# Performance work log

Hardware: AMD Instinct MI355X
Metric: run time of the kernel (lower is better)

## Reference

```python
import jax, jax.numpy as jnp
import numpy as np
from jax import lax

C = 768
CA = C // 4  # adapter_channels = 192
L = 197      # 1 CLS + 14*14 patches
T_FRAMES = 16
B = 16
N = B * T_FRAMES


def quick_gelu(x):
    return x * jax.nn.sigmoid(1.702 * x)


def setup_inputs() -> dict:
    key = jax.random.key(0)
    ks = jax.random.split(key, 16)
    s = 0.02
    return {
        "x": jax.random.normal(ks[0], (L, N, C), dtype=jnp.float32),
        "T": T_FRAMES,
        # main path (fc1 -> depthwise conv1d over T -> fc2)
        "fc1_w": jax.random.normal(ks[1], (C, CA), jnp.float32) * s,
        "fc1_b": jnp.zeros((CA,), jnp.float32),
        "conv_w": jax.random.normal(ks[2], (CA, 1, 3), jnp.float32) * s,  # (O, I/g, K)
        "conv_b": jnp.zeros((CA,), jnp.float32),
        "fc2_w": jax.random.normal(ks[3], (CA, C), jnp.float32) * s,
        "fc2_b": jnp.zeros((C,), jnp.float32),
        # offset adapter (fc1 -> depthwise conv3d (1,3,3) -> fc2)
        "off_fc1_w": jax.random.normal(ks[4], (C, CA), jnp.float32) * s,
        "off_fc1_b": jnp.zeros((CA,), jnp.float32),
        "off_conv_w": jax.random.normal(ks[5], (CA, 1, 1, 3, 3), jnp.float32) * s,  # (O, I/g, D, H, W)
        "off_conv_b": jnp.zeros((CA,), jnp.float32),
        "off_fc2_w": jax.random.normal(ks[6], (CA, C), jnp.float32) * s,
        "off_fc2_b": jnp.zeros((C,), jnp.float32),
        # mlp branch (c_in -> QuickGELU -> c_out)
        "mlp_in_w": jax.random.normal(ks[7], (C, CA), jnp.float32) * s,
        "mlp_in_b": jnp.zeros((CA,), jnp.float32),
        "mlp_out_w": jax.random.normal(ks[8], (CA, C), jnp.float32) * s,
        "mlp_out_b": jnp.zeros((C,), jnp.float32),
    }


def _offset_adapter(x, T, fc1_w, fc1_b, conv_w, conv_b, fc2_w, fc2_b):
    Lx, Nx, Cx = x.shape
    Bx = Nx // T
    HW = Lx - 1
    H = int(round(HW ** 0.5))
    Ca = fc1_w.shape[1]
    xp = jnp.transpose(x, (1, 0, 2))            # (N, L, C)
    xs = xp[:, 1:, :].reshape(Bx, T, HW, Cx)    # (B, T, HW, C)
    # former frame: index [0, 0, 1, ..., T-2]
    x_former = jnp.concatenate([xs[:, :1], xs[:, :-1]], axis=1)
    off = xs - x_former
    off = off @ fc1_w + fc1_b                   # (B, T, HW, Ca)
    off = off.reshape(Bx, T, H, H, Ca).transpose(0, 4, 1, 2, 3)  # (B, Ca, T, H, W)
    off = lax.conv_general_dilated(
        off, conv_w, window_strides=(1, 1, 1),
        padding=[(0, 0), (1, 1), (1, 1)],
        dimension_numbers=("NCDHW", "OIDHW", "NCDHW"),
        feature_group_count=Ca,
    ) + conv_b[None, :, None, None, None]
    off = off.transpose(0, 2, 3, 4, 1).reshape(Nx, HW, Ca)
    off = off @ fc2_w + fc2_b                   # (N, L-1, C)
    return jnp.transpose(off, (1, 0, 2))        # (L-1, N, C)


def reference(x, T, fc1_w, fc1_b, conv_w, conv_b, fc2_w, fc2_b,
              off_fc1_w, off_fc1_b, off_conv_w, off_conv_b, off_fc2_w, off_fc2_b,
              mlp_in_w, mlp_in_b, mlp_out_w, mlp_out_b):
    Lx, Nx, Cx = x.shape
    Bx = Nx // T
    Ca = fc1_w.shape[1]

    offset = _offset_adapter(x, T, off_fc1_w, off_fc1_b, off_conv_w, off_conv_b,
                             off_fc2_w, off_fc2_b)  # (L-1, N, C)

    # mlp identity branch
    x_id = quick_gelu(x @ mlp_in_w + mlp_in_b) @ mlp_out_w + mlp_out_b  # (L, N, C)

    # main branch: fc1 -> depthwise conv1d along T -> fc2
    h = x @ fc1_w + fc1_b                                   # (L, N, Ca)
    h = jnp.transpose(h, (1, 0, 2)).reshape(Bx, T, Lx, Ca)  # (B, T, L, Ca)
    h = h.transpose(0, 2, 3, 1).reshape(Bx * Lx, Ca, T)     # (B*L, Ca, T)
    h = lax.conv_general_dilated(
        h, conv_w, window_strides=(1,), padding=[(1, 1)],
        dimension_numbers=("NCH", "OIH", "NCH"),
        feature_group_count=Ca,
    ) + conv_b[None, :, None]
    h = h.transpose(0, 2, 1).reshape(Bx, Lx, T, Ca)
    h = h.transpose(0, 2, 1, 3).reshape(Nx, Lx, Ca)
    h = jnp.transpose(h, (1, 0, 2))                         # (L, N, Ca)
    h = h @ fc2_w + fc2_b                                   # (L, N, C)

    x_id = x_id.at[1:].add(offset)
    return h + x_id
```

## Files before the change

kernel.cpp:

```cpp
#include <hip/hip_runtime.h>

#define L_DIM 197
#define N_DIM 256
#define C_DIM 768
#define CA_DIM 192
#define M_DIM (L_DIM * N_DIM)

typedef short s16x8 __attribute__((ext_vector_type(8)));
typedef float f32x4 __attribute__((ext_vector_type(4)));

__device__ __forceinline__ unsigned short f2bf(float f) {
  unsigned x = __builtin_bit_cast(unsigned, f);
  x = (x + 0x7fffu + ((x >> 16) & 1u)) >> 16;
  return (unsigned short)x;
}
__device__ __forceinline__ float bflo(unsigned u) { return __builtin_bit_cast(float, u << 16); }
__device__ __forceinline__ float bfhi(unsigned u) { return __builtin_bit_cast(float, u & 0xffff0000u); }

__device__ __forceinline__ void unp8(uint4 v, float* f) {
  f[0] = bflo(v.x); f[1] = bfhi(v.x); f[2] = bflo(v.y); f[3] = bfhi(v.y);
  f[4] = bflo(v.z); f[5] = bfhi(v.z); f[6] = bflo(v.w); f[7] = bfhi(v.w);
}

__device__ __forceinline__ void mfma16(f32x4& acc, s16x8 a, s16x8 b) {
  asm("v_mfma_f32_16x16x32_bf16 %0, %1, %2, %0" : "+v"(acc) : "v"(a), "v"(b));
}

typedef const void __attribute__((address_space(1)))* gp_t;
typedef void __attribute__((address_space(3)))* lp_t;
__device__ __forceinline__ void gl16(const void* g, void* l) {
  __builtin_amdgcn_global_load_lds((gp_t)g, (lp_t)l, 16, 0, 0);
}

__device__ __forceinline__ int swz(int pid, int nwg) {
  const int q = nwg >> 3, r = nwg & 7, x = pid & 7, s = pid >> 3;
  return (x < r ? x * (q + 1) : r * (q + 1) + (x - r) * q) + s;
}

__global__ __launch_bounds__(256) void prep_k(
    const float* __restrict__ fc1_w, const float* __restrict__ mlp_in_w,
    const float* __restrict__ off_fc1_w, const float* __restrict__ fc2_w,
    const float* __restrict__ mlp_out_w, const float* __restrict__ off_fc2_w,
    unsigned short* __restrict__ wa, unsigned short* __restrict__ wc) {
  __shared__ float t[32][33];
  const int b = blockIdx.x;
  const int job = b / 144, tt = b - job * 144;
  const float* in = job == 0 ? fc1_w : job == 1 ? mlp_in_w : job == 2 ? off_fc1_w
                  : job == 3 ? fc2_w : job == 4 ? mlp_out_w : off_fc2_w;
  const int Cc = job < 3 ? 192 : 768;
  const int tc = Cc >> 5;
  const int tr0 = (tt / tc) << 5, tc0 = (tt - (tt / tc) * tc) << 5;
  const int lr = threadIdx.x >> 5, lc = threadIdx.x & 31;
#pragma unroll
  for (int p = 0; p < 4; p++)
    t[p * 8 + lr][lc] = in[(tr0 + p * 8 + lr) * Cc + tc0 + lc];
  __syncthreads();
#pragma unroll
  for (int p = 0; p < 4; p++) {
    const int orow = tc0 + p * 8 + lr;
    const int ocol = tr0 + lc;
    const unsigned short v = f2bf(t[lc][p * 8 + lr]);
    if (job < 3) wa[(job * 192 + orow) * 768 + ocol] = v;
    else         wc[orow * 576 + (job - 3) * 192 + ocol] = v;
  }
}

__global__ __launch_bounds__(256) void xcvt_k(const float* __restrict__ x,
                                              unsigned short* __restrict__ xb) {
  const int total8 = M_DIM * C_DIM / 8;
  const int step = gridDim.x * 256;
  for (int i = blockIdx.x * 256 + threadIdx.x; i < total8; i += step) {
    const float4 a = *(const float4*)(x + (size_t)i * 8);
    const float4 b = *(const float4*)(x + (size_t)i * 8 + 4);
    s16x8 v;
    v[0] = (short)f2bf(a.x); v[1] = (short)f2bf(a.y);
    v[2] = (short)f2bf(a.z); v[3] = (short)f2bf(a.w);
    v[4] = (short)f2bf(b.x); v[5] = (short)f2bf(b.y);
    v[6] = (short)f2bf(b.z); v[7] = (short)f2bf(b.w);
    *(s16x8*)(xb + (size_t)i * 8) = v;
  }
}

__global__ __launch_bounds__(256, 1) void gemm_a_k(
    const unsigned short* __restrict__ xb, const unsigned short* __restrict__ wa,
    const float* __restrict__ fc1_b, const float* __restrict__ mlp_in_b,
    const float* __restrict__ cw, const float* __restrict__ cb,
    const float* __restrict__ off_b1, unsigned short* __restrict__ hcat) {
  __shared__ unsigned short As[2][128 * 32];
  __shared__ unsigned short Bs[2][192 * 32];
  const int tid = threadIdx.x, lane = tid & 63, w = tid >> 6;
  const int lid = swz(blockIdx.x, 3 * 394);
  const int by = lid / 3, bx = lid - by * 3;
  const int m0 = by * 128, n0 = bx * 192;

  const int sr = tid >> 2, sc = (tid & 3) * 8;
  const unsigned short* gA0 = xb + (size_t)(m0 + sr) * C_DIM + sc;
  const unsigned short* gA1 = xb + (size_t)(m0 + 64 + sr) * C_DIM + sc;
  const unsigned short* gB = wa + (size_t)(n0 + sr) * C_DIM + sc;

  auto stage = [&](int kt, int b) {
    gl16(gA0 + kt * 32, &As[b][sr * 32 + sc]);
    gl16(gA1 + kt * 32, &As[b][(64 + sr) * 32 + sc]);
    const unsigned short* pb = gB + kt * 32;
    gl16(pb,               &Bs[b][sr * 32 + sc]);
    gl16(pb + 64 * C_DIM,  &Bs[b][(64 + sr) * 32 + sc]);
    gl16(pb + 128 * C_DIM, &Bs[b][(128 + sr) * 32 + sc]);
  };

  f32x4 acc[4][6];
#pragma unroll
  for (int i = 0; i < 4; i++)
#pragma unroll
    for (int j = 0; j < 6; j++) acc[i][j] = (f32x4){0.f, 0.f, 0.f, 0.f};

  const int fr = lane & 15, fq = lane >> 4;
  const int wm = (w >> 1) * 64, wn = (w & 1) * 96;

  stage(0, 0);
  __syncthreads();
  for (int kt = 0; kt < 24; ++kt) {
    const int b = kt & 1;
    if (kt + 1 < 24) stage(kt + 1, b ^ 1);
    s16x8 af[4], bfv[6];
#pragma unroll
    for (int mi = 0; mi < 4; mi++)
      af[mi] = *(const s16x8*)&As[b][(wm + mi * 16 + fr) * 32 + fq * 8];
#pragma unroll
    for (int ni = 0; ni < 6; ni++)
      bfv[ni] = *(const s16x8*)&Bs[b][(wn + ni * 16 + fr) * 32 + fq * 8];
#pragma unroll
    for (int mi = 0; mi < 4; mi++)
#pragma unroll
      for (int ni = 0; ni < 6; ni++) mfma16(acc[mi][ni], af[mi], bfv[ni]);
    __syncthreads();
  }

  if (bx == 0) {
#pragma unroll
    for (int ni = 0; ni < 6; ni++) {
      const int ca = wn + ni * 16 + fr;
      const float bv = fc1_b[ca];
      const float w0 = cw[ca * 3], w1 = cw[ca * 3 + 1], w2 = cw[ca * 3 + 2];
      const float cbv = cb[ca];
#pragma unroll
      for (int mi = 0; mi < 4; mi++) {
        const float v0 = acc[mi][ni][0] + bv, v1 = acc[mi][ni][1] + bv;
        const float v2 = acc[mi][ni][2] + bv, v3 = acc[mi][ni][3] + bv;
        const float pv3 = __shfl_up(v3, 16);
        const float nv0 = __shfl_down(v0, 16);
        const float p0 = fq > 0 ? pv3 : 0.f;
        const float n3 = fq < 3 ? nv0 : 0.f;
        const int mb = m0 + wm + mi * 16 + fq * 4;
        hcat[(size_t)(mb + 0) * 576 + ca] = f2bf(w0 * p0 + w1 * v0 + w2 * v1 + cbv);
        hcat[(size_t)(mb + 1) * 576 + ca] = f2bf(w0 * v0 + w1 * v1 + w2 * v2 + cbv);
        hcat[(size_t)(mb + 2) * 576 + ca] = f2bf(w0 * v1 + w1 * v2 + w2 * v3 + cbv);
        hcat[(size_t)(mb + 3) * 576 + ca] = f2bf(w0 * v2 + w1 * v3 + w2 * n3 + cbv);
      }
    }
  } else if (bx == 1) {
#pragma unroll
    for (int ni = 0; ni < 6; ni++) {
      const int ca = wn + ni * 16 + fr;
      const float bv = mlp_in_b[ca];
#pragma unroll
      for (int mi = 0; mi < 4; mi++)
#pragma unroll
        for (int r = 0; r < 4; r++) {
          const int m = m0 + wm + mi * 16 + fq * 4 + r;
          float v = acc[mi][ni][r] + bv;
          v = v / (1.f + __expf(-1.702f * v));
          hcat[(size_t)m * 576 + 192 + ca] = f2bf(v);
        }
    }
  } else {
#pragma unroll
    for (int ni = 0; ni < 6; ni++) {
      const int ca = wn + ni * 16 + fr;
      const float bv = off_b1[ca];
#pragma unroll
      for (int mi = 0; mi < 4; mi++) {
        const float v0 = acc[mi][ni][0], v1 = acc[mi][ni][1];
        const float v2 = acc[mi][ni][2], v3 = acc[mi][ni][3];
        const float pv3 = __shfl_up(v3, 16);
        const int mb = m0 + wm + mi * 16 + fq * 4;
        const float o0 = (fq == 0) ? bv : (v0 - pv3 + bv);
        hcat[(size_t)(mb + 0) * 576 + 384 + ca] = f2bf(o0);
        hcat[(size_t)(mb + 1) * 576 + 384 + ca] = f2bf(v1 - v0 + bv);
        hcat[(size_t)(mb + 2) * 576 + 384 + ca] = f2bf(v2 - v1 + bv);
        hcat[(size_t)(mb + 3) * 576 + 384 + ca] = f2bf(v3 - v2 + bv);
      }
    }
  }
}

__global__ __launch_bounds__(256) void conv3d_k(
    const float* __restrict__ w3, const float* __restrict__ b2,
    unsigned short* __restrict__ hcat) {
  __shared__ float ds[196 * 48];
  __shared__ float w3s[9 * 48];
  __shared__ float b2s[48];
  const int blk = blockIdx.x;
  const int n = blk >> 2, q = blk & 3;
  const int ch0 = q * 48;
  const int tid = threadIdx.x;

  for (int j = tid; j < 432; j += 256) {
    const int c = j / 9, tap = j % 9;
    w3s[tap * 48 + c] = w3[(ch0 + c) * 9 + tap];
  }
  if (tid < 48) b2s[tid] = b2[ch0 + tid];

  for (int j = tid; j < 196 * 6; j += 256) {
    const int hw = j / 6, ck = j % 6;
    float dv[8];
    unp8(*(const uint4*)(hcat + ((size_t)(1 + hw) * 256 + n) * 576 + 384 + ch0 + ck * 8), dv);
#pragma unroll
    for (int e = 0; e < 8; e++) ds[hw * 48 + ck * 8 + e] = dv[e];
  }
  __syncthreads();

  for (int j = tid; j < 196 * 6; j += 256) {
    const int hw = j / 6, ck = j % 6;
    const int i = hw / 14, j0 = hw - i * 14;
    float acc[8];
#pragma unroll
    for (int e = 0; e < 8; e++) acc[e] = b2s[ck * 8 + e];
#pragma unroll
    for (int di = 0; di < 3; di++) {
      const int ii = i + di - 1;
      if (ii < 0 || ii >= 14) continue;
#pragma unroll
      for (int dj = 0; dj < 3; dj++) {
        const int jc = j0 + dj - 1;
        if (jc < 0 || jc >= 14) continue;
        const float* dp = &ds[(ii * 14 + jc) * 48 + ck * 8];
        const float* wp = &w3s[(di * 3 + dj) * 48 + ck * 8];
#pragma unroll
        for (int e = 0; e < 8; e++) acc[e] += wp[e] * dp[e];
      }
    }
    unsigned o[4];
#pragma unroll
    for (int e = 0; e < 8; e += 2)
      o[e / 2] = (unsigned)f2bf(acc[e]) | ((unsigned)f2bf(acc[e + 1]) << 16);
    uint4 ov; ov.x = o[0]; ov.y = o[1]; ov.z = o[2]; ov.w = o[3];
    *(uint4*)(hcat + ((size_t)(1 + hw) * 256 + n) * 576 + 384 + ch0 + ck * 8) = ov;
  }
}

__global__ __launch_bounds__(256) void zfill_k(unsigned short* __restrict__ hcat) {
  const int idx = blockIdx.x * 256 + threadIdx.x;
  const int m = idx / 24, ch = idx - (idx / 24) * 24;
  s16x8 z = (s16x8){0, 0, 0, 0, 0, 0, 0, 0};
  *(s16x8*)&hcat[(size_t)m * 576 + 384 + ch * 8] = z;
}

__global__ __launch_bounds__(256, 1) void gemm_c_k(
    const unsigned short* __restrict__ hcat, const unsigned short* __restrict__ wc,
    const float* __restrict__ fc2_b, const float* __restrict__ mlp_out_b,
    const float* __restrict__ off_fc2_b, float* __restrict__ out) {
  __shared__ unsigned short As[2][128 * 32];
  __shared__ unsigned short Bs[2][128 * 32];
  const int tid = threadIdx.x, lane = tid & 63, w = tid >> 6;
  const int lid = swz(blockIdx.x, 6 * 394);
  const int by = lid / 6, bx = lid - by * 6;
  const int m0 = by * 128, n0 = bx * 128;

  const int srow = w * 32 + (lane >> 2), sc = (lane & 3) << 3;
  const unsigned short* gA = hcat + (size_t)(m0 + srow) * 576 + sc;
  const unsigned short* gB = wc + (size_t)(n0 + srow) * 576 + sc;
  auto stage = [&](int kt, int b) {
#pragma unroll
    for (int j = 0; j < 2; j++) {
      gl16(gA + kt * 32 + j * 16 * 576, &As[b][(srow + j * 16) * 32 + sc]);
      gl16(gB + kt * 32 + j * 16 * 576, &Bs[b][(srow + j * 16) * 32 + sc]);
    }
  };

  f32x4 acc[4][4];
#pragma unroll
  for (int i = 0; i < 4; i++)
#pragma unroll
    for (int j = 0; j < 4; j++) acc[i][j] = (f32x4){0.f, 0.f, 0.f, 0.f};

  const int fr = lane & 15, fq = lane >> 4;
  const int wm = (w >> 1) * 64, wn = (w & 1) * 64;

  stage(0, 0);
  __syncthreads();
  for (int kt = 0; kt < 18; ++kt) {
    const int b = kt & 1;
    if (kt + 1 < 18) stage(kt + 1, b ^ 1);
    s16x8 af[4], bfv[4];
#pragma unroll
    for (int mi = 0; mi < 4; mi++)
      af[mi] = *(const s16x8*)&As[b][(wm + mi * 16 + fr) * 32 + fq * 8];
#pragma unroll
    for (int ni = 0; ni < 4; ni++)
      bfv[ni] = *(const s16x8*)&Bs[b][(wn + ni * 16 + fr) * 32 + fq * 8];
#pragma unroll
    for (int mi = 0; mi < 4; mi++)
#pragma unroll
      for (int ni = 0; ni < 4; ni++) mfma16(acc[mi][ni], af[mi], bfv[ni]);
    __syncthreads();
  }

  float bv[4];
#pragma unroll
  for (int ni = 0; ni < 4; ni++) {
    const int c = n0 + wn + ni * 16 + fr;
    bv[ni] = fc2_b[c] + mlp_out_b[c] + (by >= 2 ? off_fc2_b[c] : 0.f);
  }
#pragma unroll
  for (int mi = 0; mi < 4; mi++)
#pragma unroll
    for (int r = 0; r < 4; r++) {
      const int m = m0 + wm + mi * 16 + fq * 4 + r;
      float* op = out + (size_t)m * C_DIM + n0 + wn;
#pragma unroll
      for (int ni = 0; ni < 4; ni++) op[ni * 16 + fr] = acc[mi][ni][r] + bv[ni];
    }
}

extern "C" void kernel_launch(void* const* d_in, const int* in_sizes, int n_in,
                              void* d_out, int out_size, void* d_ws, size_t ws_size,
                              hipStream_t stream) {
  const float* x          = (const float*)d_in[0];
  const float* fc1_w      = (const float*)d_in[2];
  const float* fc1_b      = (const float*)d_in[3];
  const float* conv_w     = (const float*)d_in[4];
  const float* conv_b     = (const float*)d_in[5];
  const float* fc2_w      = (const float*)d_in[6];
  const float* fc2_b      = (const float*)d_in[7];
  const float* off_fc1_w  = (const float*)d_in[8];
  const float* off_fc1_b  = (const float*)d_in[9];
  const float* off_conv_w = (const float*)d_in[10];
  const float* off_conv_b = (const float*)d_in[11];
  const float* off_fc2_w  = (const float*)d_in[12];
  const float* off_fc2_b  = (const float*)d_in[13];
  const float* mlp_in_w   = (const float*)d_in[14];
  const float* mlp_in_b   = (const float*)d_in[15];
  const float* mlp_out_w  = (const float*)d_in[16];
  const float* mlp_out_b  = (const float*)d_in[17];
  float* out = (float*)d_out;

  char* ws = (char*)d_ws;
  unsigned short* xb   = (unsigned short*)(ws);
  unsigned short* hcat = (unsigned short*)(ws + (size_t)M_DIM * C_DIM * 2);
  unsigned short* wa   = (unsigned short*)(ws + (size_t)M_DIM * C_DIM * 2
                                              + (size_t)M_DIM * 576 * 2);
  unsigned short* wc   = wa + (size_t)576 * 768;

  prep_k<<<864, 256, 0, stream>>>(fc1_w, mlp_in_w, off_fc1_w, fc2_w, mlp_out_w,
                                  off_fc2_w, wa, wc);
  xcvt_k<<<2048, 256, 0, stream>>>(x, xb);
  gemm_a_k<<<1182, 256, 0, stream>>>(xb, wa, fc1_b, mlp_in_b, conv_w, conv_b,
                                     off_fc1_b, hcat);
  zfill_k<<<24, 256, 0, stream>>>(hcat);
  conv3d_k<<<1024, 256, 0, stream>>>(off_conv_w, off_conv_b, hcat);
  gemm_c_k<<<2364, 256, 0, stream>>>(hcat, wc, fc2_b, mlp_out_b, off_fc2_b, out);
}
```

Baseline: 219.6 us.

## Triple-buffer GEMM LDS stages with vmcnt waits and fold zero-fill into GEMM A

Both GEMM kernels move from a double-buffered LDS pipeline with two __syncthreads per iteration to a three-stage ring. Each iteration does one s_barrier after a partial vmcnt wait, so the next tile's global-to-LDS loads overlap the current MFMA work. The separate zfill kernel is dropped, and the offset-branch epilogue of gemm_a now writes zeros for the first rows itself, saving a launch. The cost is more LDS per block, and correctness now depends on the hand-counted vmcnt values and on the single barrier being enough to guard buffer reuse.

```diff
diff --git a/kernel.cpp b/kernel.cpp
--- a/kernel.cpp
+++ b/kernel.cpp
@@ -31,6 +31,8 @@
 __device__ __forceinline__ void gl16(const void* g, void* l) {
   __builtin_amdgcn_global_load_lds((gp_t)g, (lp_t)l, 16, 0, 0);
 }
+
+#define WAITVM(n) asm volatile("s_waitcnt vmcnt(" #n ")" ::: "memory")
 
 __device__ __forceinline__ int swz(int pid, int nwg) {
   const int q = nwg >> 3, r = nwg & 7, x = pid & 7, s = pid >> 3;
@@ -86,8 +88,8 @@
     const float* __restrict__ fc1_b, const float* __restrict__ mlp_in_b,
     const float* __restrict__ cw, const float* __restrict__ cb,
     const float* __restrict__ off_b1, unsigned short* __restrict__ hcat) {
-  __shared__ unsigned short As[2][128 * 32];
-  __shared__ unsigned short Bs[2][192 * 32];
+  __shared__ unsigned short As[3][128 * 32];
+  __shared__ unsigned short Bs[3][192 * 32];
   const int tid = threadIdx.x, lane = tid & 63, w = tid >> 6;
   const int lid = swz(blockIdx.x, 3 * 394);
   const int by = lid / 3, bx = lid - by * 3;
@@ -117,10 +119,13 @@
   const int wm = (w >> 1) * 64, wn = (w & 1) * 96;
 
   stage(0, 0);
-  __syncthreads();
+#pragma unroll 3
   for (int kt = 0; kt < 24; ++kt) {
-    const int b = kt & 1;
-    if (kt + 1 < 24) stage(kt + 1, b ^ 1);
+    const int b = kt % 3;
+    if (kt + 1 < 24) { stage(kt + 1, (kt + 1) % 3); WAITVM(5); }
+    else             { WAITVM(0); }
+    __builtin_amdgcn_s_barrier();
+    asm volatile("" ::: "memory");
     s16x8 af[4], bfv[6];
 #pragma unroll
     for (int mi = 0; mi < 4; mi++)
@@ -132,7 +137,6 @@
     for (int mi = 0; mi < 4; mi++)
 #pragma unroll
       for (int ni = 0; ni < 6; ni++) mfma16(acc[mi][ni], af[mi], bfv[ni]);
-    __syncthreads();
   }
 
   if (bx == 0) {
@@ -173,6 +177,7 @@
         }
     }
   } else {
+    const bool zrow = (by < 2);
 #pragma unroll
     for (int ni = 0; ni < 6; ni++) {
       const int ca = wn + ni * 16 + fr;
@@ -184,10 +189,17 @@
         const float pv3 = __shfl_up(v3, 16);
         const int mb = m0 + wm + mi * 16 + fq * 4;
         const float o0 = (fq == 0) ? bv : (v0 - pv3 + bv);
-        hcat[(size_t)(mb + 0) * 576 + 384 + ca] = f2bf(o0);
-        hcat[(size_t)(mb + 1) * 576 + 384 + ca] = f2bf(v1 - v0 + bv);
-        hcat[(size_t)(mb + 2) * 576 + 384 + ca] = f2bf(v2 - v1 + bv);
-        hcat[(size_t)(mb + 3) * 576 + 384 + ca] = f2bf(v3 - v2 + bv);
+        if (zrow) {
+          hcat[(size_t)(mb + 0) * 576 + 384 + ca] = 0;
+          hcat[(size_t)(mb + 1) * 576 + 384 + ca] = 0;
+          hcat[(size_t)(mb + 2) * 576 + 384 + ca] = 0;
+          hcat[(size_t)(mb + 3) * 576 + 384 + ca] = 0;
+        } else {
+          hcat[(size_t)(mb + 0) * 576 + 384 + ca] = f2bf(o0);
+          hcat[(size_t)(mb + 1) * 576 + 384 + ca] = f2bf(v1 - v0 + bv);
+          hcat[(size_t)(mb + 2) * 576 + 384 + ca] = f2bf(v2 - v1 + bv);
+          hcat[(size_t)(mb + 3) * 576 + 384 + ca] = f2bf(v3 - v2 + bv);
+        }
       }
     }
   }
@@ -248,19 +260,12 @@
   }
 }
 
-__global__ __launch_bounds__(256) void zfill_k(unsigned short* __restrict__ hcat) {
-  const int idx = blockIdx.x * 256 + threadIdx.x;
-  const int m = idx / 24, ch = idx - (idx / 24) * 24;
-  s16x8 z = (s16x8){0, 0, 0, 0, 0, 0, 0, 0};
-  *(s16x8*)&hcat[(size_t)m * 576 + 384 + ch * 8] = z;
-}
-
 __global__ __launch_bounds__(256, 1) void gemm_c_k(
     const unsigned short* __restrict__ hcat, const unsigned short* __restrict__ wc,
     const float* __restrict__ fc2_b, const float* __restrict__ mlp_out_b,
     const float* __restrict__ off_fc2_b, float* __restrict__ out) {
-  __shared__ unsigned short As[2][128 * 32];
-  __shared__ unsigned short Bs[2][128 * 32];
+  __shared__ unsigned short As[3][128 * 32];
+  __shared__ unsigned short Bs[3][128 * 32];
   const int tid = threadIdx.x, lane = tid & 63, w = tid >> 6;
   const int lid = swz(blockIdx.x, 6 * 394);
   const int by = lid / 6, bx = lid - by * 6;
@@ -287,10 +292,13 @@
   const int wm = (w >> 1) * 64, wn = (w & 1) * 64;
 
   stage(0, 0);
-  __syncthreads();
+#pragma unroll 3
   for (int kt = 0; kt < 18; ++kt) {
-    const int b = kt & 1;
-    if (kt + 1 < 18) stage(kt + 1, b ^ 1);
+    const int b = kt % 3;
+    if (kt + 1 < 18) { stage(kt + 1, (kt + 1) % 3); WAITVM(4); }
+    else             { WAITVM(0); }
+    __builtin_amdgcn_s_barrier();
+    asm volatile("" ::: "memory");
     s16x8 af[4], bfv[4];
 #pragma unroll
     for (int mi = 0; mi < 4; mi++)
@@ -302,7 +310,6 @@
     for (int mi = 0; mi < 4; mi++)
 #pragma unroll
       for (int ni = 0; ni < 4; ni++) mfma16(acc[mi][ni], af[mi], bfv[ni]);
-    __syncthreads();
   }
 
   float bv[4];
@@ -356,7 +363,6 @@
   xcvt_k<<<2048, 256, 0, stream>>>(x, xb);
   gemm_a_k<<<1182, 256, 0, stream>>>(xb, wa, fc1_b, mlp_in_b, conv_w, conv_b,
                                      off_fc1_b, hcat);
-  zfill_k<<<24, 256, 0, stream>>>(hcat);
   conv3d_k<<<1024, 256, 0, stream>>>(off_conv_w, off_conv_b, hcat);
   gemm_c_k<<<2364, 256, 0, stream>>>(hcat, wc, fc2_b, mlp_out_b, off_fc2_b, out);
 }
```

After: 217.0 us. No clear change (-1.2%).
